# Kernel tuning notes

Measured on AMD Instinct MI355X. Metric: run time of the kernel, lower is better.

Reference implementation:

```python
import jax, jax.numpy as jnp
import numpy as np
import math

D_MODEL = 1024
N_HEADS = 16
HEAD_DIM = 64
BATCH = 2
SEQ = 2048


def setup_inputs() -> dict:
    key = jax.random.key(0)
    ks = jax.random.split(key, 5)
    x = jax.random.normal(ks[0], (BATCH, SEQ, D_MODEL), dtype=jnp.float32)
    s = 0.02
    wq = jax.random.normal(ks[1], (D_MODEL, D_MODEL), dtype=jnp.float32) * s
    wk = jax.random.normal(ks[2], (D_MODEL, D_MODEL), dtype=jnp.float32) * s
    wv = jax.random.normal(ks[3], (D_MODEL, D_MODEL), dtype=jnp.float32) * s
    wo = jax.random.normal(ks[4], (D_MODEL, D_MODEL), dtype=jnp.float32) * s
    gammas = jnp.linspace(0.9, 0.99, N_HEADS, dtype=jnp.float32)
    return {"x": x, "wq": wq, "wk": wk, "wv": wv, "wo": wo, "gammas": gammas}


def _decay_mask(length: int, gammas: jnp.ndarray, dtype) -> jnp.ndarray:
    # [H, L, L]: gamma^(t-s) for t >= s, else 0 (causal exponential decay)
    pos = jnp.arange(length)
    diff = pos[:, None] - pos[None, :]
    causal = diff >= 0
    d = jnp.maximum(diff, 0).astype(dtype)
    g = gammas.astype(dtype)[:, None, None]
    return jnp.where(causal[None], jnp.power(g, d[None]), jnp.zeros((), dtype))


def reference(x, wq, wk, wv, wo, gammas):
    B, L, D = x.shape
    H, hd = N_HEADS, HEAD_DIM
    # torch nn.Linear: y = x @ W.T
    q = (x @ wq.T).reshape(B, L, H, hd)
    k = (x @ wk.T).reshape(B, L, H, hd)
    v = (x @ wv.T).reshape(B, L, H, hd)
    scale = 1.0 / math.sqrt(hd)
    scores = jnp.einsum('bthd,bshd->bhts', q * scale, k)  # [B,H,L,L]
    decay = _decay_mask(L, gammas, x.dtype)               # [H,L,L]
    weights = scores * decay[None]
    retained = jnp.einsum('bhts,bshd->bthd', weights, v)  # [B,L,H,hd]
    return retained.reshape(B, L, H * hd) @ wo.T
```

## Files before the change

### kernel.cpp

```cpp
#include <hip/hip_runtime.h>


typedef __attribute__((ext_vector_type(8))) short bf16x8;
typedef __attribute__((ext_vector_type(4))) float f32x4;
typedef __attribute__((ext_vector_type(16))) float f32x16;
typedef __attribute__((ext_vector_type(4))) unsigned short u16x4;
typedef __attribute__((ext_vector_type(8))) unsigned short u16x8;
typedef __attribute__((ext_vector_type(4))) unsigned int u32x4;

__device__ inline unsigned short f2bf(float f) {
    unsigned int u;
    __builtin_memcpy(&u, &f, 4);
    u += 0x7fffu + ((u >> 16) & 1u);
    return (unsigned short)(u >> 16);
}
__device__ inline float bf2f(unsigned short us) {
    unsigned int u = (unsigned int)us << 16;
    float f;
    __builtin_memcpy(&f, &u, 4);
    return f;
}

__device__ inline f32x4 mfma16(bf16x8 a, bf16x8 b, f32x4 c) {
    return __builtin_amdgcn_mfma_f32_16x16x32_bf16(a, b, c, 0, 0, 0);
}
__device__ inline f32x16 mfma32(bf16x8 a, bf16x8 b, f32x16 c) {
    return __builtin_amdgcn_mfma_f32_32x32x16_bf16(a, b, c, 0, 0, 0);
}

__device__ inline void gl16(const unsigned short* g, unsigned short* l) {
    __builtin_amdgcn_global_load_lds(
        (const __attribute__((address_space(1))) unsigned int*)g,
        (__attribute__((address_space(3))) unsigned int*)l,
        16, 0, 0);
}

__device__ inline unsigned cvtpk(float lo, float hi) {
    unsigned r;
    asm("v_cvt_pk_bf16_f32 %0, %1, %2" : "=v"(r) : "v"(lo), "v"(hi));
    return r;
}

__global__ __launch_bounds__(256) void convert_bf16(
    const float* __restrict__ x,
    const float* __restrict__ wq, const float* __restrict__ wk,
    const float* __restrict__ wv, const float* __restrict__ wo,
    unsigned short* __restrict__ xb,
    unsigned short* __restrict__ wqb, unsigned short* __restrict__ wkb,
    unsigned short* __restrict__ wvb, unsigned short* __restrict__ wob)
{
    int cid = blockIdx.x * 256 + threadIdx.x;
    #pragma unroll
    for (int it = 0; it < 4; ++it, cid += 262144) {
        const float* src;
        unsigned short* dst;
        size_t off;
        if (cid < 524288) {
            src = x; dst = xb; off = (size_t)cid * 8;
        } else {
            const int t = cid - 524288;
            const int seg = t >> 17;
            off = (size_t)(t & 131071) * 8;
            src = seg == 0 ? wq : seg == 1 ? wk : seg == 2 ? wv : wo;
            dst = seg == 0 ? wqb : seg == 1 ? wkb : seg == 2 ? wvb : wob;
        }
        f32x4 a = *(const f32x4*)(src + off);
        f32x4 b = *(const f32x4*)(src + off + 4);
        u32x4 v = { cvtpk(a[0], a[1]), cvtpk(a[2], a[3]),
                    cvtpk(b[0], b[1]), cvtpk(b[2], b[3]) };
        *(u32x4*)(dst + off) = v;
    }
}

__global__ __launch_bounds__(256) void qkv_bf16(
    const unsigned short* __restrict__ xb,
    const unsigned short* __restrict__ wqb, const unsigned short* __restrict__ wkb,
    const unsigned short* __restrict__ wvb, const float* __restrict__ gammas,
    unsigned short* __restrict__ qfr, unsigned short* __restrict__ kfr,
    unsigned short* __restrict__ vfr, unsigned short* __restrict__ kftr)
{
    __shared__ unsigned short sR[128 * 64];
    __shared__ unsigned short sL[128 * 64];

    const int z = blockIdx.z;
    const unsigned short* W = (z == 0) ? wqb : (z == 1) ? wkb : wvb;
    const unsigned short* Rs = (z < 2) ? xb : W;
    const unsigned short* Ls = (z < 2) ? W : xb;
    const int rblk = (z < 2) ? blockIdx.x : blockIdx.y;
    const int lblk = (z < 2) ? blockIdx.y : blockIdx.x;

    const int tid = threadIdx.x;
    const int l = tid & 63, w = tid >> 6;
    const int lrow = l & 15, koff4 = (l >> 4) * 4;
    const int swz = lrow & 7;
    const int wrow = (w >> 1) * 64, wcol = (w & 1) * 64;

    f32x4 acc[4][4] = {};

    const int srow = w * 32 + (l >> 3);
    const int scol = ((l & 7) ^ ((l >> 3) & 7)) * 8;
    const unsigned short* gR = Rs + (size_t)(rblk * 128 + srow) * 1024 + scol;
    const unsigned short* gL = Ls + (size_t)(lblk * 128 + srow) * 1024 + scol;
    unsigned short* lRb = sR + (w * 32) * 64;
    unsigned short* lLb = sL + (w * 32) * 64;

    auto stage = [&](int kk) {
        #pragma unroll
        for (int p = 0; p < 4; ++p) {
            gl16(gR + (size_t)p * 8 * 1024 + kk, lRb + p * 512);
            gl16(gL + (size_t)p * 8 * 1024 + kk, lLb + p * 512);
        }
    };

    stage(0);
    for (int kk = 0; kk < 1024; kk += 64) {
        asm volatile("s_waitcnt vmcnt(0)" ::: "memory");
        __builtin_amdgcn_s_barrier();
        __builtin_amdgcn_sched_barrier(0);

        bf16x8 aL[2][4], bR[2][4];
        #pragma unroll
        for (int kt = 0; kt < 2; ++kt)
            #pragma unroll
            for (int f = 0; f < 4; ++f) {
                const int co = ((kt * 4 + (l >> 4)) ^ swz) * 8;
                aL[kt][f] = *(const bf16x8*)&sL[(wcol + f * 16 + lrow) * 64 + co];
                bR[kt][f] = *(const bf16x8*)&sR[(wrow + f * 16 + lrow) * 64 + co];
            }
        asm volatile("s_waitcnt lgkmcnt(0)" ::: "memory");
        __builtin_amdgcn_sched_barrier(0);
        __builtin_amdgcn_s_barrier();
        __builtin_amdgcn_sched_barrier(0);

        if (kk + 64 < 1024) stage(kk + 64);

        __builtin_amdgcn_s_setprio(1);
        #pragma unroll
        for (int kt = 0; kt < 2; ++kt)
            #pragma unroll
            for (int af = 0; af < 4; ++af)
                #pragma unroll
                for (int bf = 0; bf < 4; ++bf)
                    acc[af][bf] = mfma16(aL[kt][af], bR[kt][bf], acc[af][bf]);
        __builtin_amdgcn_s_setprio(0);
    }

    #pragma unroll
    for (int af = 0; af < 4; ++af) {
        #pragma unroll
        for (int bf = 0; bf < 4; ++bf) {
            const int m = rblk * 128 + wrow + bf * 16 + lrow;
            const int n0 = lblk * 128 + wcol + af * 16 + koff4;
            f32x4 v = acc[af][bf];
            unsigned p0 = cvtpk(v[0], v[1]), p1 = cvtpk(v[2], v[3]);
            u16x4 val = { (unsigned short)(p0 & 0xffff), (unsigned short)(p0 >> 16),
                          (unsigned short)(p1 & 0xffff), (unsigned short)(p1 >> 16) };
            if (z < 2) {
                const int bq = m >> 11, s = m & 2047;
                const int h2 = n0 >> 6, dd = n0 & 63;
                const size_t addr = (size_t)((bq * 16 + h2) * 64 + (s >> 5)) * 2048
                                  + (size_t)(dd >> 4) * 512 + (size_t)((dd >> 3) & 1) * 256
                                  + (size_t)(s & 31) * 8 + (dd & 7);
                unsigned short* dst = z ? kfr : qfr;
                *(u16x4*)(dst + addr) = val;
                if (z == 1) {
                    const float lgh = log2f(gammas[h2 & 15]);
                    const float fac = exp2f(lgh * (float)(64 - (s & 63)));
                    const size_t kb2 = (size_t)((bq * 16 + h2) * 64 + (s >> 5)) * 2048
                                     + (size_t)((s >> 4) & 1) * 512
                                     + (size_t)((s >> 3) & 1) * 256 + (s & 7);
                    #pragma unroll
                    for (int q4 = 0; q4 < 4; ++q4) {
                        const int dk = dd + q4;
                        kftr[kb2 + (size_t)(dk >> 5) * 1024 + (size_t)(dk & 31) * 8] =
                            f2bf(v[q4] * fac);
                    }
                }
            } else {
                const int h2 = m >> 6, dd = m & 63;
                const int bq = n0 >> 11, t = n0 & 2047;
                const size_t addr = (size_t)((bq * 16 + h2) * 64 + (t >> 5)) * 2048
                                  + (size_t)((dd >> 5) * 2 + ((t >> 4) & 1)) * 512
                                  + (size_t)((t >> 3) & 1) * 256
                                  + (size_t)(dd & 31) * 8 + (t & 7);
                *(u16x4*)(vfr + addr) = val;
            }
        }
    }
}

__global__ __launch_bounds__(128) void chunk_local(
    const unsigned short* __restrict__ qfr, const unsigned short* __restrict__ kfr,
    const unsigned short* __restrict__ vfr, const unsigned short* __restrict__ kft,
    const float* __restrict__ gammas, unsigned short* __restrict__ ret,
    unsigned short* __restrict__ states)
{
    const int bid = blockIdx.x;
    const int bh = bid & 31, c = bid >> 5;
    const int b = bh >> 4, h = bh & 15;
    const float lg = log2f(gammas[h]);

    const int tid = threadIdx.x;
    const int l = tid & 63, w = tid >> 6;
    const int l31 = l & 31, hi = l >> 5;

    const size_t hbase = (size_t)((b * 16 + h) * 64) * 2048;
    const unsigned short* qfb = qfr + hbase + l * 8;
    const unsigned short* kfb = kfr + hbase + l * 8;
    const unsigned short* vfb = vfr + hbase + l * 8;
    const unsigned short* ktb = kft + hbase + l * 8;

    const int gt = 2 * c + w;

    bf16x8 qf[4];
    #pragma unroll
    for (int kt = 0; kt < 4; ++kt)
        qf[kt] = *(const bf16x8*)(qfb + (size_t)gt * 2048 + kt * 512);

    float cf[16];
    #pragma unroll
    for (int r = 0; r < 16; ++r) {
        const int crow = (r & 3) + (hi << 2) + ((r >> 2) << 3);
        cf[r] = exp2f((float)(31 - crow) * lg);
    }

    f32x16 acc0 = {}, acc1 = {};
    for (int sl = 0; sl <= w; ++sl) {
        const int gs = 2 * c + sl;
        bf16x8 kc[4], vc[4];
        #pragma unroll
        for (int kt = 0; kt < 4; ++kt)
            kc[kt] = *(const bf16x8*)(kfb + (size_t)gs * 2048 + kt * 512);
        #pragma unroll
        for (int i = 0; i < 4; ++i)
            vc[i] = *(const bf16x8*)(vfb + (size_t)gs * 2048 + i * 512);

        f32x16 sc = {};
        #pragma unroll
        for (int kt = 0; kt < 4; ++kt) sc = mfma32(kc[kt], qf[kt], sc);

        const float rowf = 0.125f * exp2f((float)((w - sl) * 32 + l31 - 31) * lg);
        float wv_[16];
        if (sl == w) {
            #pragma unroll
            for (int r = 0; r < 16; ++r) {
                const int crow = (r & 3) + (hi << 2) + ((r >> 2) << 3);
                float t_ = sc[r] * rowf * cf[r];
                wv_[r] = (l31 >= crow) ? t_ : 0.0f;
            }
        } else {
            #pragma unroll
            for (int r = 0; r < 16; ++r) wv_[r] = sc[r] * rowf * cf[r];
        }
        unsigned pk_[8];
        #pragma unroll
        for (int i = 0; i < 8; ++i) pk_[i] = cvtpk(wv_[2 * i], wv_[2 * i + 1]);
        asm("v_permlane32_swap_b32 %0, %1" : "+v"(pk_[0]), "+v"(pk_[2]));
        asm("v_permlane32_swap_b32 %0, %1" : "+v"(pk_[1]), "+v"(pk_[3]));
        asm("v_permlane32_swap_b32 %0, %1" : "+v"(pk_[4]), "+v"(pk_[6]));
        asm("v_permlane32_swap_b32 %0, %1" : "+v"(pk_[5]), "+v"(pk_[7]));
        u32x4 f0v = { pk_[0], pk_[1], pk_[2], pk_[3] };
        u32x4 f1v = { pk_[4], pk_[5], pk_[6], pk_[7] };
        const bf16x8 pa0 = __builtin_bit_cast(bf16x8, f0v);
        const bf16x8 pa1 = __builtin_bit_cast(bf16x8, f1v);
        acc0 = mfma32(pa0, vc[0], acc0);
        acc0 = mfma32(pa1, vc[1], acc0);
        acc1 = mfma32(pa0, vc[2], acc1);
        acc1 = mfma32(pa1, vc[3], acc1);
    }
    #pragma unroll
    for (int r = 0; r < 16; ++r) {
        const int tl = (r & 3) + (hi << 2) + ((r >> 2) << 3);
        unsigned short* dst = ret + (size_t)(b * 2048 + gt * 32 + tl) * 1024 + h * 64 + l31;
        dst[0]  = f2bf(acc0[r]);
        dst[32] = f2bf(acc1[r]);
    }

    f32x16 as0 = {}, as1 = {};
    #pragma unroll
    for (int sl = 0; sl < 2; ++sl) {
        const int gs = 2 * c + sl;
        bf16x8 vc[4];
        #pragma unroll
        for (int i = 0; i < 4; ++i)
            vc[i] = *(const bf16x8*)(vfb + (size_t)gs * 2048 + i * 512);
        bf16x8 kt0 = *(const bf16x8*)(ktb + (size_t)gs * 2048 + (w * 2 + 0) * 512);
        bf16x8 kt1 = *(const bf16x8*)(ktb + (size_t)gs * 2048 + (w * 2 + 1) * 512);
        as0 = mfma32(kt0, vc[0], as0);
        as0 = mfma32(kt1, vc[1], as0);
        as1 = mfma32(kt0, vc[2], as1);
        as1 = mfma32(kt1, vc[3], as1);
    }
    unsigned short* sbase = states + (size_t)(bh * 32 + c) * 4096;
    #pragma unroll
    for (int r = 0; r < 16; ++r) {
        const int crow = (r & 3) + (hi << 2) + ((r >> 2) << 3);
        const size_t a = (size_t)(2 * w + (crow >> 4)) * 1024
                       + (size_t)((crow >> 3) & 1) * 256 + (crow & 7) + (size_t)l31 * 8;
        sbase[a]       = f2bf(as0[r]);
        sbase[a + 512] = f2bf(as1[r]);
    }
}

__global__ __launch_bounds__(256) void state_scan(
    unsigned short* __restrict__ states, const float* __restrict__ gammas)
{
    const int bh = blockIdx.x;
    const float g64 = exp2f(64.0f * log2f(gammas[bh & 15]));
    unsigned short* base = states + (size_t)bh * 32 * 4096 + threadIdx.x * 16;

    float S[16] = {};
    u16x8 a0 = *(const u16x8*)(base);
    u16x8 a1 = *(const u16x8*)(base + 8);
    for (int c = 0; c < 32; ++c) {
        u16x8 n0, n1;
        if (c + 1 < 32) {
            n0 = *(const u16x8*)(base + (size_t)(c + 1) * 4096);
            n1 = *(const u16x8*)(base + (size_t)(c + 1) * 4096 + 8);
        }
        u16x8 o0, o1;
        #pragma unroll
        for (int e = 0; e < 8; ++e) {
            S[e] = S[e] * g64 + bf2f(a0[e]);
            o0[e] = f2bf(S[e]);
        }
        #pragma unroll
        for (int e = 0; e < 8; ++e) {
            S[8 + e] = S[8 + e] * g64 + bf2f(a1[e]);
            o1[e] = f2bf(S[8 + e]);
        }
        *(u16x8*)(base + (size_t)c * 4096) = o0;
        *(u16x8*)(base + (size_t)c * 4096 + 8) = o1;
        a0 = n0; a1 = n1;
    }
}

__global__ __launch_bounds__(64) void inter_apply(
    const unsigned short* __restrict__ qfr, const unsigned short* __restrict__ states,
    const float* __restrict__ gammas, unsigned short* __restrict__ ret)
{
    const int bid = blockIdx.x;
    const int bh = bid & 31;
    const int c = 1 + (bid >> 5);
    const int b = bh >> 4, h = bh & 15;
    const float lg = log2f(gammas[h]);

    const int l = threadIdx.x, l31 = l & 31, hi = l >> 5;

    const unsigned short* sb_ = states + (size_t)(bh * 32 + c - 1) * 4096 + l * 8;
    bf16x8 sf[4][2];
    #pragma unroll
    for (int kt = 0; kt < 4; ++kt)
        #pragma unroll
        for (int dh = 0; dh < 2; ++dh)
            sf[kt][dh] = *(const bf16x8*)(sb_ + kt * 1024 + dh * 512);

    const size_t hbase = (size_t)((b * 16 + h) * 64) * 2048;
    const unsigned short* qfb = qfr + hbase + l * 8;

    float cfac[16];
    #pragma unroll
    for (int r = 0; r < 16; ++r) {
        const int crow = (r & 3) + (hi << 2) + ((r >> 2) << 3);
        cfac[r] = 0.125f * exp2f((float)crow * lg);
    }
    const float g32 = exp2f(32.0f * lg);

    #pragma unroll
    for (int ti = 0; ti < 2; ++ti) {
        const int gt = 2 * c + ti;
        bf16x8 qf[4];
        #pragma unroll
        for (int kt = 0; kt < 4; ++kt)
            qf[kt] = *(const bf16x8*)(qfb + (size_t)gt * 2048 + kt * 512);
        f32x16 a0 = {}, a1 = {};
        #pragma unroll
        for (int kt = 0; kt < 4; ++kt) {
            a0 = mfma32(qf[kt], sf[kt][0], a0);
            a1 = mfma32(qf[kt], sf[kt][1], a1);
        }
        const float tf = ti ? g32 : 1.0f;
        #pragma unroll
        for (int r = 0; r < 16; ++r) {
            const int tl = (r & 3) + (hi << 2) + ((r >> 2) << 3);
            const float sfac = cfac[r] * tf;
            unsigned short* dst = ret + (size_t)(b * 2048 + gt * 32 + tl) * 1024 + h * 64 + l31;
            dst[0]  = f2bf(bf2f(dst[0])  + a0[r] * sfac);
            dst[32] = f2bf(bf2f(dst[32]) + a1[r] * sfac);
        }
    }
}

__global__ __launch_bounds__(256) void out_bf16(
    const unsigned short* __restrict__ ret, const unsigned short* __restrict__ wob,
    float* __restrict__ out)
{
    __shared__ unsigned short sR[128 * 64];
    __shared__ unsigned short sL[128 * 64];

    const int rblk = blockIdx.x;
    const int lblk = blockIdx.y;

    const int tid = threadIdx.x;
    const int l = tid & 63, w = tid >> 6;
    const int lrow = l & 15, koff4 = (l >> 4) * 4;
    const int swz = lrow & 7;
    const int wrow = (w >> 1) * 64, wcol = (w & 1) * 64;

    f32x4 acc[4][4] = {};

    const int srow = w * 32 + (l >> 3);
    const int scol = ((l & 7) ^ ((l >> 3) & 7)) * 8;
    const unsigned short* gR = ret + (size_t)(rblk * 128 + srow) * 1024 + scol;
    const unsigned short* gL = wob + (size_t)(lblk * 128 + srow) * 1024 + scol;
    unsigned short* lRb = sR + (w * 32) * 64;
    unsigned short* lLb = sL + (w * 32) * 64;

    auto stage = [&](int kk) {
        #pragma unroll
        for (int p = 0; p < 4; ++p) {
            gl16(gR + (size_t)p * 8 * 1024 + kk, lRb + p * 512);
            gl16(gL + (size_t)p * 8 * 1024 + kk, lLb + p * 512);
        }
    };

    stage(0);
    for (int kk = 0; kk < 1024; kk += 64) {
        asm volatile("s_waitcnt vmcnt(0)" ::: "memory");
        __builtin_amdgcn_s_barrier();
        __builtin_amdgcn_sched_barrier(0);

        bf16x8 aL[2][4], bR[2][4];
        #pragma unroll
        for (int kt = 0; kt < 2; ++kt)
            #pragma unroll
            for (int f = 0; f < 4; ++f) {
                const int co = ((kt * 4 + (l >> 4)) ^ swz) * 8;
                aL[kt][f] = *(const bf16x8*)&sL[(wcol + f * 16 + lrow) * 64 + co];
                bR[kt][f] = *(const bf16x8*)&sR[(wrow + f * 16 + lrow) * 64 + co];
            }
        asm volatile("s_waitcnt lgkmcnt(0)" ::: "memory");
        __builtin_amdgcn_sched_barrier(0);
        __builtin_amdgcn_s_barrier();
        __builtin_amdgcn_sched_barrier(0);

        if (kk + 64 < 1024) stage(kk + 64);

        __builtin_amdgcn_s_setprio(1);
        #pragma unroll
        for (int kt = 0; kt < 2; ++kt)
            #pragma unroll
            for (int af = 0; af < 4; ++af)
                #pragma unroll
                for (int bf = 0; bf < 4; ++bf)
                    acc[af][bf] = mfma16(aL[kt][af], bR[kt][bf], acc[af][bf]);
        __builtin_amdgcn_s_setprio(0);
    }

    #pragma unroll
    for (int af = 0; af < 4; ++af)
        #pragma unroll
        for (int bf = 0; bf < 4; ++bf) {
            const int m = rblk * 128 + wrow + bf * 16 + lrow;
            const int n0 = lblk * 128 + wcol + af * 16 + koff4;
            *(f32x4*)(out + (size_t)m * 1024 + n0) = acc[af][bf];
        }
}

extern "C" void kernel_launch(void* const* d_in, const int* in_sizes, int n_in,
                              void* d_out, int out_size, void* d_ws, size_t ws_size,
                              hipStream_t stream) {
    const float* x      = (const float*)d_in[0];
    const float* wq     = (const float*)d_in[1];
    const float* wk     = (const float*)d_in[2];
    const float* wv     = (const float*)d_in[3];
    const float* wo     = (const float*)d_in[4];
    const float* gammas = (const float*)d_in[5];
    float* out = (float*)d_out;

    unsigned short* ws = (unsigned short*)d_ws;
    const size_t M = 1024 * 1024;
    unsigned short* qf     = ws;
    unsigned short* kf     = ws + 4 * M;
    unsigned short* vf     = ws + 8 * M;
    unsigned short* ret    = ws + 12 * M;
    unsigned short* xb     = ret;
    unsigned short* wqb    = ws + 16 * M;
    unsigned short* wkb    = ws + 17 * M;
    unsigned short* wvb    = ws + 18 * M;
    unsigned short* states = ws + 16 * M;
    unsigned short* kft    = ws + 20 * M;
    unsigned short* wob    = ws + 24 * M;

    convert_bf16<<<1024, 256, 0, stream>>>(x, wq, wk, wv, wo, xb, wqb, wkb, wvb, wob);
    qkv_bf16<<<dim3(32, 8, 3), 256, 0, stream>>>(xb, wqb, wkb, wvb, gammas,
                                                 qf, kf, vf, kft);
    chunk_local<<<1024, 128, 0, stream>>>(qf, kf, vf, kft, gammas, ret, states);
    state_scan<<<32, 256, 0, stream>>>(states, gammas);
    inter_apply<<<992, 64, 0, stream>>>(qf, states, gammas, ret);
    out_bf16<<<dim3(32, 8), 256, 0, stream>>>(ret, wob, out);
}
```

Baseline: 95.89 us.

## Split chunk state computation from output, fuse inter-chunk apply into chunk output

New measurement: 86.14 us (median of 2 runs). 1.11x faster.

```diff
diff --git a/kernel.cpp b/kernel.cpp
--- a/kernel.cpp
+++ b/kernel.cpp
@@ -75,9 +75,9 @@
 __global__ __launch_bounds__(256) void qkv_bf16(
     const unsigned short* __restrict__ xb,
     const unsigned short* __restrict__ wqb, const unsigned short* __restrict__ wkb,
-    const unsigned short* __restrict__ wvb, const float* __restrict__ gammas,
+    const unsigned short* __restrict__ wvb,
     unsigned short* __restrict__ qfr, unsigned short* __restrict__ kfr,
-    unsigned short* __restrict__ vfr, unsigned short* __restrict__ kftr)
+    unsigned short* __restrict__ vfr)
 {
     __shared__ unsigned short sR[128 * 64];
     __shared__ unsigned short sL[128 * 64];
@@ -163,19 +163,6 @@
                                   + (size_t)(s & 31) * 8 + (dd & 7);
                 unsigned short* dst = z ? kfr : qfr;
                 *(u16x4*)(dst + addr) = val;
-                if (z == 1) {
-                    const float lgh = log2f(gammas[h2 & 15]);
-                    const float fac = exp2f(lgh * (float)(64 - (s & 63)));
-                    const size_t kb2 = (size_t)((bq * 16 + h2) * 64 + (s >> 5)) * 2048
-                                     + (size_t)((s >> 4) & 1) * 512
-                                     + (size_t)((s >> 3) & 1) * 256 + (s & 7);
-                    #pragma unroll
-                    for (int q4 = 0; q4 < 4; ++q4) {
-                        const int dk = dd + q4;
-                        kftr[kb2 + (size_t)(dk >> 5) * 1024 + (size_t)(dk & 31) * 8] =
-                            f2bf(v[q4] * fac);
-                    }
-                }
             } else {
                 const int h2 = m >> 6, dd = m & 63;
                 const int bq = n0 >> 11, t = n0 & 2047;
@@ -189,33 +176,158 @@
     }
 }
 
-__global__ __launch_bounds__(128) void chunk_local(
-    const unsigned short* __restrict__ qfr, const unsigned short* __restrict__ kfr,
-    const unsigned short* __restrict__ vfr, const unsigned short* __restrict__ kft,
-    const float* __restrict__ gammas, unsigned short* __restrict__ ret,
-    unsigned short* __restrict__ states)
-{
+__global__ __launch_bounds__(128) void a_state(
+    const unsigned short* __restrict__ kfr, const unsigned short* __restrict__ vfr,
+    const float* __restrict__ gammas, unsigned short* __restrict__ states)
+{
+    __shared__ unsigned short kbuf[4096];
+
     const int bid = blockIdx.x;
     const int bh = bid & 31, c = bid >> 5;
     const int b = bh >> 4, h = bh & 15;
     const float lg = log2f(gammas[h]);
+    const float gi1 = exp2f(-lg);
 
     const int tid = threadIdx.x;
     const int l = tid & 63, w = tid >> 6;
     const int l31 = l & 31, hi = l >> 5;
+
+    const size_t hbase = (size_t)((b * 16 + h) * 64) * 2048;
+    const unsigned short* src = kfr + hbase + (size_t)c * 4096;
+    #pragma unroll
+    for (int p = 0; p < 4; ++p)
+        gl16(src + (w * 4 + p) * 512 + l * 8, kbuf + (w * 4 + p) * 512 + l * 8);
+    asm volatile("s_waitcnt vmcnt(0)" ::: "memory");
+    __builtin_amdgcn_s_barrier();
+    __builtin_amdgcn_sched_barrier(0);
+
+    const unsigned short* vfb = vfr + hbase + l * 8;
+    const int dd = 32 * w + l31;
+    const int dbase = (dd >> 4) * 512 + ((dd >> 3) & 1) * 256 + (dd & 7);
+
+    f32x16 as0 = {}, as1 = {};
+    #pragma unroll
+    for (int sl = 0; sl < 2; ++sl) {
+        bf16x8 vc[4];
+        #pragma unroll
+        for (int i = 0; i < 4; ++i)
+            vc[i] = *(const bf16x8*)(vfb + (size_t)(2 * c + sl) * 2048 + i * 512);
+        bf16x8 kt[2];
+        #pragma unroll
+        for (int kti = 0; kti < 2; ++kti) {
+            float fac = exp2f(lg * (float)(64 - (32 * sl + 16 * kti + 8 * hi)));
+            unsigned pk[4];
+            #pragma unroll
+            for (int jj = 0; jj < 4; ++jj) {
+                const int s0 = 16 * kti + 8 * hi + 2 * jj;
+                float e0 = bf2f(kbuf[sl * 2048 + dbase + s0 * 8]) * fac;
+                fac *= gi1;
+                float e1 = bf2f(kbuf[sl * 2048 + dbase + (s0 + 1) * 8]) * fac;
+                fac *= gi1;
+                pk[jj] = cvtpk(e0, e1);
+            }
+            u32x4 kv_ = { pk[0], pk[1], pk[2], pk[3] };
+            kt[kti] = __builtin_bit_cast(bf16x8, kv_);
+        }
+        as0 = mfma32(kt[0], vc[0], as0);
+        as0 = mfma32(kt[1], vc[1], as0);
+        as1 = mfma32(kt[0], vc[2], as1);
+        as1 = mfma32(kt[1], vc[3], as1);
+    }
+
+    unsigned short* sbase = states + (size_t)(bh * 32 + c) * 4096;
+    #pragma unroll
+    for (int r = 0; r < 16; ++r) {
+        const int crow = (r & 3) + (hi << 2) + ((r >> 2) << 3);
+        const size_t a = (size_t)(2 * w + (crow >> 4)) * 1024
+                       + (size_t)((crow >> 3) & 1) * 256 + (crow & 7) + (size_t)l31 * 8;
+        sbase[a]       = f2bf(as0[r]);
+        sbase[a + 512] = f2bf(as1[r]);
+    }
+}
+
+__global__ __launch_bounds__(256) void state_scan(
+    unsigned short* __restrict__ states, const float* __restrict__ gammas)
+{
+    const int bh = blockIdx.x;
+    const float g64 = exp2f(64.0f * log2f(gammas[bh & 15]));
+    unsigned short* base = states + (size_t)bh * 32 * 4096 + threadIdx.x * 16;
+
+    float S[16] = {};
+    u16x8 a0 = *(const u16x8*)(base);
+    u16x8 a1 = *(const u16x8*)(base + 8);
+    for (int c = 0; c < 32; ++c) {
+        u16x8 n0, n1;
+        if (c + 1 < 32) {
+            n0 = *(const u16x8*)(base + (size_t)(c + 1) * 4096);
+            n1 = *(const u16x8*)(base + (size_t)(c + 1) * 4096 + 8);
+        }
+        u16x8 o0, o1;
+        #pragma unroll
+        for (int e = 0; e < 8; ++e) {
+            S[e] = S[e] * g64 + bf2f(a0[e]);
+            o0[e] = f2bf(S[e]);
+        }
+        #pragma unroll
+        for (int e = 0; e < 8; ++e) {
+            S[8 + e] = S[8 + e] * g64 + bf2f(a1[e]);
+            o1[e] = f2bf(S[8 + e]);
+        }
+        *(u16x8*)(base + (size_t)c * 4096) = o0;
+        *(u16x8*)(base + (size_t)c * 4096 + 8) = o1;
+        a0 = n0; a1 = n1;
+    }
+}
+
+__global__ __launch_bounds__(128) void chunk_out(
+    const unsigned short* __restrict__ qfr, const unsigned short* __restrict__ kfr,
+    const unsigned short* __restrict__ vfr, const unsigned short* __restrict__ states,
+    const float* __restrict__ gammas, unsigned short* __restrict__ ret)
+{
+    const int bid = blockIdx.x;
+    const int bh = bid & 31, c = bid >> 5;
+    const int b = bh >> 4, h = bh & 15;
+    const float lg = log2f(gammas[h]);
+
+    const int tid = threadIdx.x;
+    const int l = tid & 63, w = tid >> 6;
+    const int l31 = l & 31, hi = l >> 5;
+    const int gt = 2 * c + w;
 
     const size_t hbase = (size_t)((b * 16 + h) * 64) * 2048;
     const unsigned short* qfb = qfr + hbase + l * 8;
     const unsigned short* kfb = kfr + hbase + l * 8;
     const unsigned short* vfb = vfr + hbase + l * 8;
-    const unsigned short* ktb = kft + hbase + l * 8;
-
-    const int gt = 2 * c + w;
 
     bf16x8 qf[4];
     #pragma unroll
     for (int kt = 0; kt < 4; ++kt)
         qf[kt] = *(const bf16x8*)(qfb + (size_t)gt * 2048 + kt * 512);
+
+    f32x16 acc0 = {}, acc1 = {};
+
+    if (c > 0) {
+        const unsigned short* sb_ = states + (size_t)(bh * 32 + c - 1) * 4096 + l * 8;
+        bf16x8 sf[4][2];
+        #pragma unroll
+        for (int kt = 0; kt < 4; ++kt)
+            #pragma unroll
+            for (int dh = 0; dh < 2; ++dh)
+                sf[kt][dh] = *(const bf16x8*)(sb_ + kt * 1024 + dh * 512);
+        f32x16 a0 = {}, a1 = {};
+        #pragma unroll
+        for (int kt = 0; kt < 4; ++kt) {
+            a0 = mfma32(qf[kt], sf[kt][0], a0);
+            a1 = mfma32(qf[kt], sf[kt][1], a1);
+        }
+        #pragma unroll
+        for (int r = 0; r < 16; ++r) {
+            const int crow = (r & 3) + (hi << 2) + ((r >> 2) << 3);
+            const float sfac = 0.125f * exp2f(lg * (float)(32 * w + crow));
+            acc0[r] = a0[r] * sfac;
+            acc1[r] = a1[r] * sfac;
+        }
+    }
 
     float cf[16];
     #pragma unroll
@@ -223,8 +335,6 @@
         const int crow = (r & 3) + (hi << 2) + ((r >> 2) << 3);
         cf[r] = exp2f((float)(31 - crow) * lg);
     }
-
-    f32x16 acc0 = {}, acc1 = {};
     for (int sl = 0; sl <= w; ++sl) {
         const int gs = 2 * c + sl;
         bf16x8 kc[4], vc[4];
@@ -268,126 +378,13 @@
         acc1 = mfma32(pa0, vc[2], acc1);
         acc1 = mfma32(pa1, vc[3], acc1);
     }
+
     #pragma unroll
     for (int r = 0; r < 16; ++r) {
         const int tl = (r & 3) + (hi << 2) + ((r >> 2) << 3);
         unsigned short* dst = ret + (size_t)(b * 2048 + gt * 32 + tl) * 1024 + h * 64 + l31;
         dst[0]  = f2bf(acc0[r]);
         dst[32] = f2bf(acc1[r]);
-    }
-
-    f32x16 as0 = {}, as1 = {};
-    #pragma unroll
-    for (int sl = 0; sl < 2; ++sl) {
-        const int gs = 2 * c + sl;
-        bf16x8 vc[4];
-        #pragma unroll
-        for (int i = 0; i < 4; ++i)
-            vc[i] = *(const bf16x8*)(vfb + (size_t)gs * 2048 + i * 512);
-        bf16x8 kt0 = *(const bf16x8*)(ktb + (size_t)gs * 2048 + (w * 2 + 0) * 512);
-        bf16x8 kt1 = *(const bf16x8*)(ktb + (size_t)gs * 2048 + (w * 2 + 1) * 512);
-        as0 = mfma32(kt0, vc[0], as0);
-        as0 = mfma32(kt1, vc[1], as0);
-        as1 = mfma32(kt0, vc[2], as1);
-        as1 = mfma32(kt1, vc[3], as1);
-    }
-    unsigned short* sbase = states + (size_t)(bh * 32 + c) * 4096;
-    #pragma unroll
-    for (int r = 0; r < 16; ++r) {
-        const int crow = (r & 3) + (hi << 2) + ((r >> 2) << 3);
-        const size_t a = (size_t)(2 * w + (crow >> 4)) * 1024
-                       + (size_t)((crow >> 3) & 1) * 256 + (crow & 7) + (size_t)l31 * 8;
-        sbase[a]       = f2bf(as0[r]);
-        sbase[a + 512] = f2bf(as1[r]);
-    }
-}
-
-__global__ __launch_bounds__(256) void state_scan(
-    unsigned short* __restrict__ states, const float* __restrict__ gammas)
-{
-    const int bh = blockIdx.x;
-    const float g64 = exp2f(64.0f * log2f(gammas[bh & 15]));
-    unsigned short* base = states + (size_t)bh * 32 * 4096 + threadIdx.x * 16;
-
-    float S[16] = {};
-    u16x8 a0 = *(const u16x8*)(base);
-    u16x8 a1 = *(const u16x8*)(base + 8);
-    for (int c = 0; c < 32; ++c) {
-        u16x8 n0, n1;
-        if (c + 1 < 32) {
-            n0 = *(const u16x8*)(base + (size_t)(c + 1) * 4096);
-            n1 = *(const u16x8*)(base + (size_t)(c + 1) * 4096 + 8);
-        }
-        u16x8 o0, o1;
-        #pragma unroll
-        for (int e = 0; e < 8; ++e) {
-            S[e] = S[e] * g64 + bf2f(a0[e]);
-            o0[e] = f2bf(S[e]);
-        }
-        #pragma unroll
-        for (int e = 0; e < 8; ++e) {
-            S[8 + e] = S[8 + e] * g64 + bf2f(a1[e]);
-            o1[e] = f2bf(S[8 + e]);
-        }
-        *(u16x8*)(base + (size_t)c * 4096) = o0;
-        *(u16x8*)(base + (size_t)c * 4096 + 8) = o1;
-        a0 = n0; a1 = n1;
-    }
-}
-
-__global__ __launch_bounds__(64) void inter_apply(
-    const unsigned short* __restrict__ qfr, const unsigned short* __restrict__ states,
-    const float* __restrict__ gammas, unsigned short* __restrict__ ret)
-{
-    const int bid = blockIdx.x;
-    const int bh = bid & 31;
-    const int c = 1 + (bid >> 5);
-    const int b = bh >> 4, h = bh & 15;
-    const float lg = log2f(gammas[h]);
-
-    const int l = threadIdx.x, l31 = l & 31, hi = l >> 5;
-
-    const unsigned short* sb_ = states + (size_t)(bh * 32 + c - 1) * 4096 + l * 8;
-    bf16x8 sf[4][2];
-    #pragma unroll
-    for (int kt = 0; kt < 4; ++kt)
-        #pragma unroll
-        for (int dh = 0; dh < 2; ++dh)
-            sf[kt][dh] = *(const bf16x8*)(sb_ + kt * 1024 + dh * 512);
-
-    const size_t hbase = (size_t)((b * 16 + h) * 64) * 2048;
-    const unsigned short* qfb = qfr + hbase + l * 8;
-
-    float cfac[16];
-    #pragma unroll
-    for (int r = 0; r < 16; ++r) {
-        const int crow = (r & 3) + (hi << 2) + ((r >> 2) << 3);
-        cfac[r] = 0.125f * exp2f((float)crow * lg);
-    }
-    const float g32 = exp2f(32.0f * lg);
-
-    #pragma unroll
-    for (int ti = 0; ti < 2; ++ti) {
-        const int gt = 2 * c + ti;
-        bf16x8 qf[4];
-        #pragma unroll
-        for (int kt = 0; kt < 4; ++kt)
-            qf[kt] = *(const bf16x8*)(qfb + (size_t)gt * 2048 + kt * 512);
-        f32x16 a0 = {}, a1 = {};
-        #pragma unroll
-        for (int kt = 0; kt < 4; ++kt) {
-            a0 = mfma32(qf[kt], sf[kt][0], a0);
-            a1 = mfma32(qf[kt], sf[kt][1], a1);
-        }
-        const float tf = ti ? g32 : 1.0f;
-        #pragma unroll
-        for (int r = 0; r < 16; ++r) {
-            const int tl = (r & 3) + (hi << 2) + ((r >> 2) << 3);
-            const float sfac = cfac[r] * tf;
-            unsigned short* dst = ret + (size_t)(b * 2048 + gt * 32 + tl) * 1024 + h * 64 + l31;
-            dst[0]  = f2bf(bf2f(dst[0])  + a0[r] * sfac);
-            dst[32] = f2bf(bf2f(dst[32]) + a1[r] * sfac);
-        }
     }
 }
 
@@ -489,14 +486,12 @@
     unsigned short* wkb    = ws + 17 * M;
     unsigned short* wvb    = ws + 18 * M;
     unsigned short* states = ws + 16 * M;
-    unsigned short* kft    = ws + 20 * M;
-    unsigned short* wob    = ws + 24 * M;
+    unsigned short* wob    = ws + 20 * M;
 
     convert_bf16<<<1024, 256, 0, stream>>>(x, wq, wk, wv, wo, xb, wqb, wkb, wvb, wob);
-    qkv_bf16<<<dim3(32, 8, 3), 256, 0, stream>>>(xb, wqb, wkb, wvb, gammas,
-                                                 qf, kf, vf, kft);
-    chunk_local<<<1024, 128, 0, stream>>>(qf, kf, vf, kft, gammas, ret, states);
+    qkv_bf16<<<dim3(32, 8, 3), 256, 0, stream>>>(xb, wqb, wkb, wvb, qf, kf, vf);
+    a_state<<<1024, 128, 0, stream>>>(kf, vf, gammas, states);
     state_scan<<<32, 256, 0, stream>>>(states, gammas);
-    inter_apply<<<992, 64, 0, stream>>>(qf, states, gammas, ret);
+    chunk_out<<<1024, 128, 0, stream>>>(qf, kf, vf, states, gammas, ret);
     out_bf16<<<dim3(32, 8), 256, 0, stream>>>(ret, wob, out);
 }
```
